# Kernel optimization log

Hardware: AMD Instinct MI355X
Metric: run time of the kernel (lower is better)

The kernel has to match this reference:

```python
import jax, jax.numpy as jnp
import numpy as np

TAU = 1.0

def setup_inputs() -> dict:
    key = jax.random.key(0)
    k1, k2 = jax.random.split(key)
    b, t, n, e, top_k = 2, 64, 1024, 512, 256
    x = jax.random.normal(k1, (b, t, n, e), dtype=jnp.float32)
    # torch nn.Linear(embed_size, top_k): weight [top_k, e], bias [top_k]
    W = jax.random.normal(k2, (top_k, e), dtype=jnp.float32) * (1.0 / np.sqrt(e))
    b_bias = jnp.zeros((top_k,), dtype=jnp.float32)
    return {"x": x, "W": W, "b_bias": b_bias}

def reference(x, W, b_bias):
    b, t, n, e = x.shape
    x_flat = x.reshape(b, t * n, e)                 # [b, m, e], m = t*n
    scores = x_flat @ W.T + b_bias                  # [b, m, top_k]
    weights = jax.nn.softmax(scores / TAU, axis=1)  # softmax over token axis m
    # weighted-sum pooling for all top_k slots at once (replaces torch loop)
    selected = jnp.einsum('bmk,bme->bke', weights, x_flat)  # [b, top_k, e]
    return selected
```

## Files before the change

### kernel.cpp

```cpp
#include <hip/hip_runtime.h>
#include <stdint.h>

#define B_DIM 2
#define M_DIM 65536
#define E_DIM 512
#define K_DIM 256

typedef __bf16 bf16_t;
typedef __bf16 bf16x8 __attribute__((ext_vector_type(8)));
typedef float  f32x4  __attribute__((ext_vector_type(4)));

typedef const __attribute__((address_space(1))) void* gas_ptr;
typedef __attribute__((address_space(3))) void* las_ptr;

__device__ __forceinline__ void async_load16(const void* g, void* l) {
    __builtin_amdgcn_global_load_lds((gas_ptr)g, (las_ptr)l, 16, 0, 0);
}

__device__ __forceinline__ unsigned short bf16_bits(float f) {
    return __builtin_bit_cast(unsigned short, (__bf16)f);
}
__device__ __forceinline__ unsigned int pack2(float lo, float hi) {
    return (unsigned int)bf16_bits(lo) | ((unsigned int)bf16_bits(hi) << 16);
}
__device__ __forceinline__ float bf16u_to_f32(unsigned short us) {
    return __builtin_bit_cast(float, (unsigned)us << 16);
}
__device__ __forceinline__ uint2 pack8_fp8(const float* f) {
    int lo = __builtin_amdgcn_cvt_pk_fp8_f32(f[0], f[1], 0, false);
    lo = __builtin_amdgcn_cvt_pk_fp8_f32(f[2], f[3], lo, true);
    int hi = __builtin_amdgcn_cvt_pk_fp8_f32(f[4], f[5], 0, false);
    hi = __builtin_amdgcn_cvt_pk_fp8_f32(f[6], f[7], hi, true);
    return make_uint2((unsigned)lo, (unsigned)hi);
}

__global__ __launch_bounds__(256) void cast_w(const float* __restrict__ W, bf16_t* __restrict__ Wb) {
    int idx = blockIdx.x * 256 + threadIdx.x;
    float4 v = ((const float4*)W)[idx];
    ((uint2*)Wb)[idx] = make_uint2(pack2(v.x, v.y), pack2(v.z, v.w));
}

__global__ __launch_bounds__(256) void gemm1_exp_t(const float* __restrict__ x, const bf16_t* __restrict__ Wb,
                                                   unsigned char* __restrict__ pb8, float* __restrict__ psums,
                                                   unsigned char* __restrict__ xT8) {
    int gid = blockIdx.x;
    int mt = gid & 1023;
    int b  = gid >> 10;
    int m0 = mt * 64;
    int t = threadIdx.x, lane = t & 63, w = t >> 6;

    __shared__ __align__(16) char smem[40960];
    bf16_t* Alds = (bf16_t*)smem;
    bf16_t* Blds = (bf16_t*)(smem + 32768);
    bf16_t* Elds = (bf16_t*)smem;

    const float* xb = x + ((size_t)b * M_DIM + m0) * E_DIM;

    f32x4 zero = {0.f, 0.f, 0.f, 0.f};
    f32x4 acc[4][4];
#pragma unroll
    for (int i = 0; i < 4; ++i)
#pragma unroll
        for (int j = 0; j < 4; ++j) acc[i][j] = zero;

    int bst_r = t >> 2, bst_s0 = t & 3;

    int q = lane >> 4, r15 = lane & 15;

    for (int ke = 0; ke < 8; ++ke) {
        int e0 = ke * 64;
#pragma unroll
        for (int is = 0; is < 8; ++is) {
            int c = is * 256 + t;
            int row = c >> 3, sl = c & 7;
            int ge = sl ^ (row & 7);
            async_load16(Wb + (size_t)row * E_DIM + e0 + ge * 8, Alds + c * 8);
        }
#pragma unroll
        for (int sg = 0; sg < 2; ++sg) {
            int sl = bst_s0 + sg * 4;
            int ge = sl ^ (bst_r & 7);
            const float4* f = (const float4*)(xb + (size_t)bst_r * E_DIM + e0 + ge * 8);
            float4 a0 = f[0], a1 = f[1];
            *(uint4*)(Blds + bst_r * 64 + sl * 8) =
                make_uint4(pack2(a0.x, a0.y), pack2(a0.z, a0.w), pack2(a1.x, a1.y), pack2(a1.z, a1.w));
        }
        __syncthreads();

#pragma unroll
        for (int h = 0; h < 2; ++h) {
            bf16x8 af[4], bfr[4];
#pragma unroll
            for (int i = 0; i < 4; ++i) {
                int r = w * 64 + i * 16 + r15;
                int sl = (h * 4 + q) ^ (r & 7);
                af[i] = *(const bf16x8*)(Alds + r * 64 + sl * 8);
            }
#pragma unroll
            for (int j = 0; j < 4; ++j) {
                int r = j * 16 + r15;
                int sl = (h * 4 + q) ^ (r & 7);
                bfr[j] = *(const bf16x8*)(Blds + r * 64 + sl * 8);
            }
#pragma unroll
            for (int i = 0; i < 4; ++i)
#pragma unroll
                for (int j = 0; j < 4; ++j)
                    acc[i][j] = __builtin_amdgcn_mfma_f32_16x16x32_bf16(af[i], bfr[j], acc[i][j], 0, 0, 0);
        }

        {
            const unsigned short* Bs = (const unsigned short*)Blds;
            int l7 = t & 7;
            int mbase = l7 * 8;
            int ebase = t >> 3;
#pragma unroll
            for (int p = 0; p < 2; ++p) {
                int ecol = p * 32 + ebase;
                float f[8];
#pragma unroll
                for (int s = 0; s < 8; ++s) {
                    int mmr = (s + l7) & 7;
                    int sl = (ecol >> 3) ^ mmr;
                    f[mmr] = bf16u_to_f32(Bs[(mbase + mmr) * 64 + sl * 8 + (ecol & 7)]);
                }
                *(uint2*)(xT8 + ((size_t)(b * E_DIM + e0 + ecol)) * M_DIM + m0 + mbase) = pack8_fp8(f);
            }
        }
        __syncthreads();
    }

    int cc = lane & 15;
    float ksum[4][4];
#pragma unroll
    for (int i = 0; i < 4; ++i)
#pragma unroll
        for (int p = 0; p < 4; ++p) ksum[i][p] = 0.f;

#pragma unroll
    for (int i = 0; i < 4; ++i) {
        int kr = w * 64 + i * 16 + q * 4;
#pragma unroll
        for (int j = 0; j < 4; ++j) {
            int colb = j * 16 + cc;
            int g = colb >> 3, off = colb & 7;
#pragma unroll
            for (int p = 0; p < 4; ++p) {
                float v = __expf(acc[i][j][p]);
                ksum[i][p] += v;
                int k = kr + p;
                Elds[k * 64 + ((g ^ (k & 7)) * 8) + off] = (bf16_t)v;
            }
        }
    }
#pragma unroll
    for (int mask = 1; mask < 16; mask <<= 1)
#pragma unroll
        for (int i = 0; i < 4; ++i)
#pragma unroll
            for (int p = 0; p < 4; ++p)
                ksum[i][p] += __shfl_xor(ksum[i][p], mask, 64);
    if (cc == 0) {
        float* pp = psums + ((size_t)b * 1024 + mt) * 256;
#pragma unroll
        for (int i = 0; i < 4; ++i)
#pragma unroll
            for (int p = 0; p < 4; ++p)
                pp[w * 64 + i * 16 + q * 4 + p] = ksum[i][p];
    }
    __syncthreads();

    {
        int g = t & 7, rsub = t >> 3;
        unsigned char* dstb = pb8 + (size_t)b * K_DIM * M_DIM + m0;
#pragma unroll
        for (int p = 0; p < 8; ++p) {
            int k = p * 32 + rsub;
            const unsigned short* src = (const unsigned short*)(Elds + k * 64 + ((g ^ (k & 7)) * 8));
            float f[8];
#pragma unroll
            for (int s = 0; s < 8; ++s) f[s] = bf16u_to_f32(src[s]);
            *(uint2*)(dstb + (size_t)k * M_DIM + g * 8) = pack8_fp8(f);
        }
    }
}

__global__ __launch_bounds__(256) void gemm2(const unsigned char* __restrict__ pb8, const unsigned char* __restrict__ xT8,
                                             float* __restrict__ part) {
    int bid = blockIdx.x;
    int kt = bid & 1, et = (bid >> 1) & 3, ch = (bid >> 3) & 31, b = bid >> 8;
    int t = threadIdx.x, lane = t & 63, w = t >> 6;
    int wk = w & 1, we = w >> 1;

    __shared__ __align__(16) unsigned char Alds[128 * 64];
    __shared__ __align__(16) unsigned char Blds[128 * 64];

    const unsigned char* Ab = pb8 + ((size_t)(b * K_DIM + kt * 128)) * M_DIM + ch * 2048;
    const unsigned char* Bb = xT8 + ((size_t)(b * E_DIM + et * 128)) * M_DIM + ch * 2048;

    f32x4 zero = {0.f, 0.f, 0.f, 0.f};
    f32x4 acc[4][4];
#pragma unroll
    for (int i = 0; i < 4; ++i)
#pragma unroll
        for (int j = 0; j < 4; ++j) acc[i][j] = zero;

    int q = lane >> 4, r15 = lane & 15;

    for (int km = 0; km < 32; ++km) {
        int m0 = km * 64;
#pragma unroll
        for (int is = 0; is < 2; ++is) {
            int c = is * 256 + t;
            int row = c >> 2, a = c & 3;
            int sr = (row & 3) ^ ((row >> 2) & 3);
            int bsl = a ^ sr;
            async_load16(Ab + (size_t)row * M_DIM + m0 + bsl * 16, Alds + c * 16);
            async_load16(Bb + (size_t)row * M_DIM + m0 + bsl * 16, Blds + c * 16);
        }
        __syncthreads();

#pragma unroll
        for (int h = 0; h < 2; ++h) {
            long av[4], bv[4];
#pragma unroll
            for (int i = 0; i < 4; ++i) {
                int r = wk * 128 / 2 * 0 + wk * 64 + i * 16 + r15;
                int sr = (r & 3) ^ ((r >> 2) & 3);
                int g = h * 4 + q;
                int off = (((g >> 1) ^ sr) * 16) + (g & 1) * 8;
                av[i] = *(const long*)(Alds + r * 64 + off);
            }
#pragma unroll
            for (int j = 0; j < 4; ++j) {
                int r = we * 64 + j * 16 + r15;
                int sr = (r & 3) ^ ((r >> 2) & 3);
                int g = h * 4 + q;
                int off = (((g >> 1) ^ sr) * 16) + (g & 1) * 8;
                bv[j] = *(const long*)(Blds + r * 64 + off);
            }
#pragma unroll
            for (int i = 0; i < 4; ++i)
#pragma unroll
                for (int j = 0; j < 4; ++j)
                    acc[i][j] = __builtin_amdgcn_mfma_f32_16x16x32_fp8_fp8(av[i], bv[j], acc[i][j], 0, 0, 0);
        }
        __syncthreads();
    }

    float* pp = part + (size_t)bid * 16384;
    int cc = lane & 15;
#pragma unroll
    for (int i = 0; i < 4; ++i)
#pragma unroll
        for (int p = 0; p < 4; ++p) {
            int kl = wk * 64 + i * 16 + q * 4 + p;
#pragma unroll
            for (int j = 0; j < 4; ++j) {
                int el = we * 64 + j * 16 + cc;
                pp[kl * 128 + el] = acc[i][j][p];
            }
        }
}

__global__ __launch_bounds__(256) void reduce_out(const float* __restrict__ part, const float* __restrict__ psums,
                                                  float* __restrict__ out) {
    int bid = blockIdx.x;
    int ehalf = bid & 1, k = (bid >> 1) & 255, b = bid >> 9;
    int t = threadIdx.x, lane = t & 63;

    float cs = 0.f;
#pragma unroll
    for (int c = 0; c < 4; ++c) {
        int mt = c * 256 + t;
        cs += psums[((size_t)b * 1024 + mt) * 256 + k];
    }
#pragma unroll
    for (int mask = 1; mask < 64; mask <<= 1) cs += __shfl_xor(cs, mask, 64);
    __shared__ float cspart[4];
    if (lane == 0) cspart[t >> 6] = cs;
    __syncthreads();
    float colsum = (cspart[0] + cspart[1]) + (cspart[2] + cspart[3]);

    int e = ehalf * 256 + t;
    int kt = k >> 7, kl = k & 127, et = e >> 7, el = e & 127;
    float s = 0.f;
#pragma unroll
    for (int ch = 0; ch < 32; ++ch) {
        int bid2 = kt | (et << 1) | (ch << 3) | (b << 8);
        s += part[(size_t)bid2 * 16384 + kl * 128 + el];
    }
    out[((size_t)(b * 256 + k)) * 512 + e] = s / colsum;
}

extern "C" void kernel_launch(void* const* d_in, const int* in_sizes, int n_in,
                              void* d_out, int out_size, void* d_ws, size_t ws_size,
                              hipStream_t stream) {
    (void)in_sizes; (void)n_in; (void)out_size; (void)ws_size;
    const float* x = (const float*)d_in[0];
    const float* W = (const float*)d_in[1];

    char* ws = (char*)d_ws;
    unsigned char* xT8 = (unsigned char*)ws;
    bf16_t* Wb    = (bf16_t*)(ws + 67108864);
    unsigned char* pb8 = (unsigned char*)(ws + 67371008);
    float*  psums = (float*)(ws + 100925440);
    float*  part  = (float*)(ws + 103022592);
    float*  out   = (float*)d_out;

    cast_w<<<128, 256, 0, stream>>>(W, Wb);
    gemm1_exp_t<<<2048, 256, 0, stream>>>(x, Wb, pb8, psums, xT8);
    gemm2<<<512, 256, 0, stream>>>(pb8, xT8, part);
    reduce_out<<<1024, 256, 0, stream>>>(part, psums, out);
}
```

Baseline: 445.4 us.

## Use 32x32x64 scaled fp8 MFMA with double-buffered LDS in gemm2

Replaces the 16x16x32 fp8 MFMA tiles in gemm2 with the gfx950 mfma_scale 32x32x64 f8f6f4 instruction, using unit scales, and rewrites the LDS fragment loads and output index mapping to match. It also double-buffers the A/B LDS tiles so the async global-to-LDS load for the next K slice is issued before the current slice is computed. This aims to cut MFMA instruction count and hide load latency, at the cost of more LDS and reliance on the 32x32 output layout being mapped correctly. There is only one barrier per iteration and no explicit wait on the async loads, which could be a race.

```diff
diff --git a/kernel.cpp b/kernel.cpp
--- a/kernel.cpp
+++ b/kernel.cpp
@@ -9,6 +9,8 @@
 typedef __bf16 bf16_t;
 typedef __bf16 bf16x8 __attribute__((ext_vector_type(8)));
 typedef float  f32x4  __attribute__((ext_vector_type(4)));
+typedef float  f32x16 __attribute__((ext_vector_type(16)));
+typedef int    i32x8  __attribute__((ext_vector_type(8)));
 
 typedef const __attribute__((address_space(1))) void* gas_ptr;
 typedef __attribute__((address_space(3))) void* las_ptr;
@@ -192,72 +194,83 @@
     int t = threadIdx.x, lane = t & 63, w = t >> 6;
     int wk = w & 1, we = w >> 1;
 
-    __shared__ __align__(16) unsigned char Alds[128 * 64];
-    __shared__ __align__(16) unsigned char Blds[128 * 64];
+    __shared__ __align__(16) unsigned char Alds[2][128 * 64];
+    __shared__ __align__(16) unsigned char Blds[2][128 * 64];
 
     const unsigned char* Ab = pb8 + ((size_t)(b * K_DIM + kt * 128)) * M_DIM + ch * 2048;
     const unsigned char* Bb = xT8 + ((size_t)(b * E_DIM + et * 128)) * M_DIM + ch * 2048;
 
-    f32x4 zero = {0.f, 0.f, 0.f, 0.f};
-    f32x4 acc[4][4];
-#pragma unroll
-    for (int i = 0; i < 4; ++i)
-#pragma unroll
-        for (int j = 0; j < 4; ++j) acc[i][j] = zero;
-
-    int q = lane >> 4, r15 = lane & 15;
-
-    for (int km = 0; km < 32; ++km) {
-        int m0 = km * 64;
+    f32x16 acc[2][2];
+#pragma unroll
+    for (int i = 0; i < 2; ++i)
+#pragma unroll
+        for (int j = 0; j < 2; ++j)
+#pragma unroll
+            for (int p = 0; p < 16; ++p) acc[i][j][p] = 0.f;
+
+    int l31 = lane & 31, g = lane >> 5;
+
+    auto STAGE = [&](int buf, int m0) {
 #pragma unroll
         for (int is = 0; is < 2; ++is) {
             int c = is * 256 + t;
             int row = c >> 2, a = c & 3;
             int sr = (row & 3) ^ ((row >> 2) & 3);
             int bsl = a ^ sr;
-            async_load16(Ab + (size_t)row * M_DIM + m0 + bsl * 16, Alds + c * 16);
-            async_load16(Bb + (size_t)row * M_DIM + m0 + bsl * 16, Blds + c * 16);
-        }
+            async_load16(Ab + (size_t)row * M_DIM + m0 + bsl * 16, &Alds[buf][c * 16]);
+            async_load16(Bb + (size_t)row * M_DIM + m0 + bsl * 16, &Blds[buf][c * 16]);
+        }
+    };
+
+    STAGE(0, 0);
+    __syncthreads();
+
+    for (int km = 0; km < 32; ++km) {
+        int cur = km & 1;
+        if (km + 1 < 32) STAGE(cur ^ 1, (km + 1) * 64);
+
+        i32x8 av[2], bv[2];
+#pragma unroll
+        for (int i = 0; i < 2; ++i) {
+            int r = wk * 64 + i * 32 + l31;
+            int sr = (r & 3) ^ ((r >> 2) & 3);
+            int4 lo = *(const int4*)(&Alds[cur][r * 64 + (((2 * g) ^ sr) * 16)]);
+            int4 hi = *(const int4*)(&Alds[cur][r * 64 + (((2 * g + 1) ^ sr) * 16)]);
+            av[i][0] = lo.x; av[i][1] = lo.y; av[i][2] = lo.z; av[i][3] = lo.w;
+            av[i][4] = hi.x; av[i][5] = hi.y; av[i][6] = hi.z; av[i][7] = hi.w;
+        }
+#pragma unroll
+        for (int j = 0; j < 2; ++j) {
+            int r = we * 64 + j * 32 + l31;
+            int sr = (r & 3) ^ ((r >> 2) & 3);
+            int4 lo = *(const int4*)(&Blds[cur][r * 64 + (((2 * g) ^ sr) * 16)]);
+            int4 hi = *(const int4*)(&Blds[cur][r * 64 + (((2 * g + 1) ^ sr) * 16)]);
+            bv[j][0] = lo.x; bv[j][1] = lo.y; bv[j][2] = lo.z; bv[j][3] = lo.w;
+            bv[j][4] = hi.x; bv[j][5] = hi.y; bv[j][6] = hi.z; bv[j][7] = hi.w;
+        }
+
+#pragma unroll
+        for (int i = 0; i < 2; ++i)
+#pragma unroll
+            for (int j = 0; j < 2; ++j)
+                acc[i][j] = __builtin_amdgcn_mfma_scale_f32_32x32x64_f8f6f4(
+                    av[i], bv[j], acc[i][j],
+                    0 , 0 ,
+                    0, 0x7f7f7f7f ,
+                    0, 0x7f7f7f7f );
+
         __syncthreads();
-
-#pragma unroll
-        for (int h = 0; h < 2; ++h) {
-            long av[4], bv[4];
-#pragma unroll
-            for (int i = 0; i < 4; ++i) {
-                int r = wk * 128 / 2 * 0 + wk * 64 + i * 16 + r15;
-                int sr = (r & 3) ^ ((r >> 2) & 3);
-                int g = h * 4 + q;
-                int off = (((g >> 1) ^ sr) * 16) + (g & 1) * 8;
-                av[i] = *(const long*)(Alds + r * 64 + off);
-            }
-#pragma unroll
-            for (int j = 0; j < 4; ++j) {
-                int r = we * 64 + j * 16 + r15;
-                int sr = (r & 3) ^ ((r >> 2) & 3);
-                int g = h * 4 + q;
-                int off = (((g >> 1) ^ sr) * 16) + (g & 1) * 8;
-                bv[j] = *(const long*)(Blds + r * 64 + off);
-            }
-#pragma unroll
-            for (int i = 0; i < 4; ++i)
-#pragma unroll
-                for (int j = 0; j < 4; ++j)
-                    acc[i][j] = __builtin_amdgcn_mfma_f32_16x16x32_fp8_fp8(av[i], bv[j], acc[i][j], 0, 0, 0);
-        }
-        __syncthreads();
     }
 
     float* pp = part + (size_t)bid * 16384;
-    int cc = lane & 15;
-#pragma unroll
-    for (int i = 0; i < 4; ++i)
-#pragma unroll
-        for (int p = 0; p < 4; ++p) {
-            int kl = wk * 64 + i * 16 + q * 4 + p;
-#pragma unroll
-            for (int j = 0; j < 4; ++j) {
-                int el = we * 64 + j * 16 + cc;
+#pragma unroll
+    for (int i = 0; i < 2; ++i)
+#pragma unroll
+        for (int p = 0; p < 16; ++p) {
+            int kl = wk * 64 + i * 32 + (p & 3) + 8 * (p >> 2) + 4 * g;
+#pragma unroll
+            for (int j = 0; j < 2; ++j) {
+                int el = we * 64 + j * 32 + l31;
                 pp[kl * 128 + el] = acc[i][j][p];
             }
         }
```

Result: no change. 444.6 us (-0.2%).
